# Performance work log

Measured on AMD Instinct MI355X. Metric: run time of the kernel, lower is better.

## Reference

```python
import jax, jax.numpy as jnp
import numpy as np
import math
from jax import lax

B, T, IN_DIM, D, H, L, OUT = 2, 2048, 128, 512, 8, 4, 128
HD = D // H
FF = int(4.0 * D)
NEG = -1e30  # stands in for -inf in the causal mask (identical softmax result)


def setup_inputs() -> dict:
    key = jax.random.key(0)
    ks = jax.random.split(key, 8)
    s = 0.02
    def p(k, shape):
        return jax.random.normal(k, shape, jnp.float32) * s
    return {
        "x": jax.random.normal(ks[0], (B, T, IN_DIM), jnp.float32),
        "Win": p(ks[1], (IN_DIM, D)), "bin_": jnp.zeros((D,), jnp.float32),
        "Wqkv": p(ks[2], (L, D, 3 * D)), "bqkv": jnp.zeros((L, 3 * D), jnp.float32),
        "Wo": p(ks[3], (L, D, D)), "bo": jnp.zeros((L, D), jnp.float32),
        "ln1_g": jnp.ones((L, D), jnp.float32), "ln1_b": jnp.zeros((L, D), jnp.float32),
        "Wf1": p(ks[4], (L, D, FF)), "bf1": jnp.zeros((L, FF), jnp.float32),
        "Wf2": p(ks[5], (L, FF, D)), "bf2": jnp.zeros((L, D), jnp.float32),
        "ln2_g": jnp.ones((L, D), jnp.float32), "ln2_b": jnp.zeros((L, D), jnp.float32),
        "lnf_g": jnp.ones((D,), jnp.float32), "lnf_b": jnp.zeros((D,), jnp.float32),
        "Wout": p(ks[6], (D, OUT)), "bout": jnp.zeros((OUT,), jnp.float32),
    }


def _layernorm(x, g, b, eps=1e-5):
    mu = jnp.mean(x, axis=-1, keepdims=True)
    var = jnp.mean(jnp.square(x - mu), axis=-1, keepdims=True)
    return (x - mu) * lax.rsqrt(var + eps) * g + b


def _sinusoidal_pe(t, d):
    pos = jnp.arange(t, dtype=jnp.float32)[:, None]
    div = jnp.exp(jnp.arange(0, d, 2, dtype=jnp.float32) * (-math.log(10000.0) / d))
    pe = jnp.zeros((t, d), jnp.float32)
    pe = pe.at[:, 0::2].set(jnp.sin(pos * div)).at[:, 1::2].set(jnp.cos(pos * div))
    return pe


def _alibi_bias():
    # ALiBi slopes (H=8 is a power of 2): start = 2**(-2**(-(log2(H)-3)))
    start = 2.0 ** (-(2.0 ** (-(math.log2(H) - 3.0))))
    slopes = jnp.array([start * (start ** i) for i in range(H)], jnp.float32)
    pos = jnp.arange(T)
    dist = jnp.triu(pos[None, :] - pos[:, None]).astype(jnp.float32)  # faithful: .triu() zeroes j<i
    bias = slopes[:, None, None] * dist  # [H,T,T]
    causal = jnp.triu(jnp.ones((T, T), bool), 1)
    return jnp.where(causal[None], NEG, bias)


def _forward(x, Win, bin_, Wqkv, bqkv, Wo, bo, ln1_g, ln1_b, Wf1, bf1, Wf2, bf2,
             ln2_g, ln2_b, lnf_g, lnf_b, Wout, bout):
    x = x @ Win + bin_                      # [B,T,D] project_in
    x = x + _sinusoidal_pe(T, D)            # internal time embedding
    bias = _alibi_bias()                    # [H,T,T]
    scale = 1.0 / math.sqrt(HD)

    def block(h, params):
        wqkv, bq, wo, bo_, g1, b1, wf1, bf1_, wf2, bf2_, g2, b2 = params
        y = _layernorm(h, g1, b1)
        qkv = y @ wqkv + bq                 # [B,T,3D]
        q, k, v = jnp.split(qkv, 3, axis=-1)
        def heads(t):
            return t.reshape(B, T, H, HD).transpose(0, 2, 1, 3)  # [B,H,T,HD]
        q, k, v = heads(q), heads(k), heads(v)
        logits = jnp.einsum('bhqd,bhkd->bhqk', q, k) * scale + bias[None]
        attn = jax.nn.softmax(logits, axis=-1)
        y = jnp.einsum('bhqk,bhkd->bhqd', attn, v)
        y = y.transpose(0, 2, 1, 3).reshape(B, T, D)
        h = h + (y @ wo + bo_)
        y = _layernorm(h, g2, b2)
        y = jax.nn.gelu(y @ wf1 + bf1_, approximate=False) @ wf2 + bf2_
        h = h + y
        return h, None

    x, _ = lax.scan(block, x, (Wqkv, bqkv, Wo, bo, ln1_g, ln1_b, Wf1, bf1, Wf2, bf2, ln2_g, ln2_b))
    x = _layernorm(x, lnf_g, lnf_b)         # final_norm
    return x @ Wout + bout                  # output head


def reference(x, Win, bin_, Wqkv, bqkv, Wo, bo, ln1_g, ln1_b, Wf1, bf1, Wf2, bf2,
              ln2_g, ln2_b, lnf_g, lnf_b, Wout, bout):
    return _forward(x, Win, bin_, Wqkv, bqkv, Wo, bo, ln1_g, ln1_b, Wf1, bf1,
                    Wf2, bf2, ln2_g, ln2_b, lnf_g, lnf_b, Wout, bout)
```

## Files before the change

kernel.cpp:

```cpp
#include <hip/hip_runtime.h>
#include <math.h>
#include <type_traits>
#include <utility>

#define TT 2048
typedef unsigned short u16;
typedef unsigned int u32;
typedef float f32x4 __attribute__((ext_vector_type(4)));
typedef float f32x16 __attribute__((ext_vector_type(16)));
typedef short s16x8 __attribute__((ext_vector_type(8)));
typedef __bf16 bf16x8 __attribute__((ext_vector_type(8)));
typedef __bf16 bf16x2 __attribute__((ext_vector_type(2)));
typedef u32 u32x4 __attribute__((ext_vector_type(4)));

enum { EPI_PE = 0, EPI_BF16 = 1, EPI_RES = 2, EPI_GELU = 3, EPI_OUTF = 4 };

template<typename V, typename = void> struct mfma_takes : std::false_type {};
template<typename V> struct mfma_takes<V, std::void_t<decltype(
    __builtin_amdgcn_mfma_f32_16x16x32_bf16(std::declval<V>(), std::declval<V>(),
                                            std::declval<f32x4>(), 0, 0, 0))>>
    : std::true_type {};

template<typename VA>
__device__ __forceinline__ f32x4 MFMA_t(VA a, VA b, f32x4 c) {
    if constexpr (mfma_takes<VA>::value) {
        return __builtin_amdgcn_mfma_f32_16x16x32_bf16(a, b, c, 0, 0, 0);
    } else {
        return __builtin_amdgcn_mfma_f32_16x16x32_bf16(
            __builtin_bit_cast(bf16x8, a), __builtin_bit_cast(bf16x8, b), c, 0, 0, 0);
    }
}

template<typename V, typename = void> struct mfma32_takes : std::false_type {};
template<typename V> struct mfma32_takes<V, std::void_t<decltype(
    __builtin_amdgcn_mfma_f32_32x32x16_bf16(std::declval<V>(), std::declval<V>(),
                                            std::declval<f32x16>(), 0, 0, 0))>>
    : std::true_type {};

template<typename VA>
__device__ __forceinline__ f32x16 MFMA32(VA a, VA b, f32x16 c) {
    if constexpr (mfma32_takes<VA>::value) {
        return __builtin_amdgcn_mfma_f32_32x32x16_bf16(a, b, c, 0, 0, 0);
    } else {
        return __builtin_amdgcn_mfma_f32_32x32x16_bf16(
            __builtin_bit_cast(bf16x8, a), __builtin_bit_cast(bf16x8, b), c, 0, 0, 0);
    }
}

__device__ __forceinline__ u16 f2b(float f) {
    u32 u = __float_as_uint(f);
    return (u16)((u + 0x7FFFu + ((u >> 16) & 1u)) >> 16);
}

__device__ __forceinline__ u32 pkbf(float a, float b) {
    bf16x2 t; t[0] = (__bf16)a; t[1] = (__bf16)b;
    return __builtin_bit_cast(u32, t);
}

__device__ __forceinline__ void gload16(const void* g, void* lds_base, int lds_byte_off) {
    __builtin_amdgcn_global_load_lds(
        (const __attribute__((address_space(1))) void*)g,
        (__attribute__((address_space(3))) void*)((char*)lds_base + lds_byte_off),
        16, 0, 0);
}

template<int EPI, int TM, int TN>
__global__ __launch_bounds__(256)
void k_gemm_mfma(const u16* __restrict__ A, const u16* __restrict__ Bt,
                 const float* __restrict__ bias, const float* __restrict__ Rf,
                 void* __restrict__ Cout, int M, int N, int K)
{
    constexpr int MF = TM / 32;
    constexpr int NF = TN / 32;
    __shared__ __attribute__((aligned(16))) u16 As[TM * 64];
    __shared__ __attribute__((aligned(16))) u16 Bs[TN * 64];
    const int tid = threadIdx.x;
    const int l = tid & 63, wv = tid >> 6;
    const int l15 = l & 15, lg = l >> 4;
    const int wr = wv >> 1, wc = wv & 1;
    const int row0 = blockIdx.y * TM, col0 = blockIdx.x * TN;

    f32x4 acc[MF][NF];
#pragma unroll
    for (int m = 0; m < MF; ++m)
#pragma unroll
        for (int n = 0; n < NF; ++n) acc[m][n] = (f32x4){0.f, 0.f, 0.f, 0.f};

    for (int kt = 0; kt < K; kt += 64) {
#pragma unroll
        for (int i = 0; i < TM / 32; ++i) {
            const int u = i * 256 + wv * 64 + l;
            const int ar = u >> 3, ac = u & 7;
            const int sc = (ac ^ (ar & 7)) << 3;
            const int off = __builtin_amdgcn_readfirstlane((i * 256 + wv * 64) * 16);
            gload16(A + (size_t)(row0 + ar) * K + kt + sc, As, off);
        }
#pragma unroll
        for (int i = 0; i < TN / 32; ++i) {
            const int u = i * 256 + wv * 64 + l;
            const int ar = u >> 3, ac = u & 7;
            const int sc = (ac ^ (ar & 7)) << 3;
            const int off = __builtin_amdgcn_readfirstlane((i * 256 + wv * 64) * 16);
            gload16(Bt + (size_t)(col0 + ar) * K + kt + sc, Bs, off);
        }
        __syncthreads();
        s16x8 af[MF][2], bf[NF][2];
#pragma unroll
        for (int m = 0; m < MF; ++m) {
            const int r = wr * (TM / 2) + m * 16 + l15;
#pragma unroll
            for (int s = 0; s < 2; ++s)
                af[m][s] = *(const s16x8*)(As + r * 64 + (((s * 4 + lg) ^ (r & 7)) << 3));
        }
#pragma unroll
        for (int n = 0; n < NF; ++n) {
            const int r = wc * (TN / 2) + n * 16 + l15;
#pragma unroll
            for (int s = 0; s < 2; ++s)
                bf[n][s] = *(const s16x8*)(Bs + r * 64 + (((s * 4 + lg) ^ (r & 7)) << 3));
        }
#pragma unroll
        for (int s = 0; s < 2; ++s)
#pragma unroll
            for (int m = 0; m < MF; ++m)
#pragma unroll
                for (int n = 0; n < NF; ++n)
                    acc[m][n] = MFMA_t(af[m][s], bf[n][s], acc[m][n]);
        __syncthreads();
    }

#pragma unroll
    for (int m = 0; m < MF; ++m)
#pragma unroll
        for (int rg = 0; rg < 4; ++rg) {
            const int row = row0 + wr * (TM / 2) + m * 16 + lg * 4 + rg;
#pragma unroll
            for (int n = 0; n < NF; ++n) {
                const int col = col0 + wc * (TN / 2) + n * 16 + l15;
                float v = acc[m][n][rg] + bias[col];
                const size_t idx = (size_t)row * N + col;
                if constexpr (EPI == EPI_PE) {
                    const int t = row & (TT - 1);
                    const float freq = __expf(-(float)(col & ~1) * 0.017988946039015984f);
                    const float ang = (float)t * freq;
                    v += (col & 1) ? cosf(ang) : sinf(ang);
                    ((float*)Cout)[idx] = v;
                } else if constexpr (EPI == EPI_BF16) {
                    ((u16*)Cout)[idx] = f2b(v);
                } else if constexpr (EPI == EPI_GELU) {
                    v = 0.5f * v * (1.f + erff(v * 0.7071067811865475f));
                    ((u16*)Cout)[idx] = f2b(v);
                } else if constexpr (EPI == EPI_RES) {
                    ((float*)Cout)[idx] = Rf[idx] + v;
                } else {
                    ((float*)Cout)[idx] = v;
                }
            }
        }
}

__global__ __launch_bounds__(256)
void k_ln(const float* __restrict__ X, const float* __restrict__ g,
          const float* __restrict__ b, u16* __restrict__ Y)
{
    const int lane = threadIdx.x & 63;
    const int row = blockIdx.x * 4 + (threadIdx.x >> 6);
    const float* x = X + (size_t)row * 512 + lane * 8;

    float4 v0 = *(const float4*)x;
    float4 v1 = *(const float4*)(x + 4);
    float vals[8] = {v0.x, v0.y, v0.z, v0.w, v1.x, v1.y, v1.z, v1.w};

    float s = 0.f;
#pragma unroll
    for (int i = 0; i < 8; ++i) s += vals[i];
#pragma unroll
    for (int off = 32; off >= 1; off >>= 1) s += __shfl_xor(s, off);
    const float mu = s * (1.f / 512.f);

    float sq = 0.f;
#pragma unroll
    for (int i = 0; i < 8; ++i) { float d = vals[i] - mu; sq += d * d; }
#pragma unroll
    for (int off = 32; off >= 1; off >>= 1) sq += __shfl_xor(sq, off);
    const float rs = rsqrtf(sq * (1.f / 512.f) + 1e-5f);

    const float* gp = g + lane * 8;
    const float* bp = b + lane * 8;
    float4 g0 = *(const float4*)gp, g1 = *(const float4*)(gp + 4);
    float4 b0 = *(const float4*)bp, b1 = *(const float4*)(bp + 4);
    float ga[8] = {g0.x, g0.y, g0.z, g0.w, g1.x, g1.y, g1.z, g1.w};
    float bb[8] = {b0.x, b0.y, b0.z, b0.w, b1.x, b1.y, b1.z, b1.w};

    u32 pk[4];
#pragma unroll
    for (int i = 0; i < 4; ++i) {
        float a0 = (vals[2 * i]     - mu) * rs * ga[2 * i]     + bb[2 * i];
        float a1 = (vals[2 * i + 1] - mu) * rs * ga[2 * i + 1] + bb[2 * i + 1];
        pk[i] = (u32)f2b(a0) | ((u32)f2b(a1) << 16);
    }
    *(uint4*)(Y + (size_t)row * 512 + lane * 8) = make_uint4(pk[0], pk[1], pk[2], pk[3]);
}

__global__ __launch_bounds__(256, 4)
void k_attn(const u16* __restrict__ qkv, const u16* __restrict__ Kf,
            const u16* __restrict__ Vf, u16* __restrict__ y)
{
    __shared__ float Om[4][32 * 65];
    __shared__ float Ml[4][32][2];
    const int tid = threadIdx.x;
    const int l = tid & 63, w = tid >> 6;
    const int l31 = l & 31, hi = l >> 5;
    const int bx = blockIdx.x;
    const int xcd = bx & 7, s = bx >> 3;
    const int bh = xcd * 2 + (s & 1);
    const int t_tile = 63 - (s >> 1);
    const int b = bh >> 3, hh = bh & 7;
    const int bT = b * TT, hh64 = hh * 64;

    const int qg = t_tile * 32 + l31;
    const int NT = (t_tile >> 1) + 1;

    f32x16 o[2] = {};
    float m = -1e30f, lsum = 0.f;

    if (w < NT) {
        s16x8 qf[4];
        {
            const u16* qsrc = qkv + (size_t)(bT + qg) * 1536 + hh64 + hi * 8;
#pragma unroll
            for (int dk = 0; dk < 4; ++dk) qf[dk] = *(const s16x8*)(qsrc + dk * 16);
        }
        const u16* kfb = Kf + ((size_t)bh * 8 + hi) * 2048 * 8;
        const u16* vfb = Vf + (((size_t)bh * 32) * 8 + hi) * 64 * 8;

        for (int g = w; g < NT; g += 4) {
            s16x8 kf[8];
#pragma unroll
            for (int nb = 0; nb < 2; ++nb)
#pragma unroll
                for (int dk = 0; dk < 4; ++dk)
                    kf[nb * 4 + dk] = *(const s16x8*)(
                        kfb + ((size_t)(dk * 2) * 2048 + g * 64 + nb * 32 + l31) * 8);

            f32x16 sA[2];
#pragma unroll
            for (int nb = 0; nb < 2; ++nb) {
                f32x16 acc = {};
#pragma unroll
                for (int dk = 0; dk < 4; ++dk) acc = MFMA32(kf[nb * 4 + dk], qf[dk], acc);
                sA[nb] = acc;
            }

            if (g == NT - 1) {
                const int kvb = g * 64, hi4 = hi * 4;
#pragma unroll
                for (int nb = 0; nb < 2; ++nb)
#pragma unroll
                    for (int r = 0; r < 16; ++r) {
                        const int kv = kvb + nb * 32 + (r & 3) + 8 * (r >> 2) + hi4;
                        sA[nb][r] = (kv > qg) ? -1e30f : sA[nb][r];
                    }
            }

            float tmp[16];
#pragma unroll
            for (int r = 0; r < 16; ++r) tmp[r] = fmaxf(sA[0][r], sA[1][r]);
#pragma unroll
            for (int st = 8; st >= 1; st >>= 1)
#pragma unroll
                for (int r = 0; r < 8; ++r)
                    if (r < st) tmp[r] = fmaxf(tmp[r], tmp[r + st]);
            float mt = fmaxf(tmp[0], __shfl_xor(tmp[0], 32));
            const bool grow = !__all(mt <= m);
            if (grow) {
                const float mn = fmaxf(m, mt);
                const float alpha = __expf((m - mn) * 0.125f);
                m = mn;
                lsum *= alpha;
#pragma unroll
                for (int dt = 0; dt < 2; ++dt)
#pragma unroll
                    for (int r = 0; r < 16; ++r) o[dt][r] *= alpha;
            }
            const float mc = -m * 0.125f;

            float p[2][16];
            float sum[16];
#pragma unroll
            for (int r = 0; r < 16; ++r) {
                p[0][r] = __expf(fmaf(sA[0][r], 0.125f, mc));
                p[1][r] = __expf(fmaf(sA[1][r], 0.125f, mc));
                sum[r] = p[0][r] + p[1][r];
            }
#pragma unroll
            for (int st = 8; st >= 1; st >>= 1)
#pragma unroll
                for (int r = 0; r < 8; ++r)
                    if (r < st) sum[r] += sum[r + st];
            float psum = sum[0] + __shfl_xor(sum[0], 32);
            lsum += psum;

            u32 pk2[2][8], sw2[2][8];
#pragma unroll
            for (int nb = 0; nb < 2; ++nb)
#pragma unroll
                for (int i = 0; i < 8; ++i) {
                    pk2[nb][i] = pkbf(p[nb][2 * i], p[nb][2 * i + 1]);
                    sw2[nb][i] = __shfl_xor(pk2[nb][i], 32);
                }
            s16x8 pa[4];
#pragma unroll
            for (int nb = 0; nb < 2; ++nb)
#pragma unroll
                for (int k16 = 0; k16 < 2; ++k16) {
                    const int i0 = k16 * 4;
                    u32 w0 = hi ? sw2[nb][i0 + 2] : pk2[nb][i0 + 0];
                    u32 w1 = hi ? sw2[nb][i0 + 3] : pk2[nb][i0 + 1];
                    u32 w2 = hi ? pk2[nb][i0 + 2] : sw2[nb][i0 + 0];
                    u32 w3 = hi ? pk2[nb][i0 + 3] : sw2[nb][i0 + 1];
                    u32x4 t4 = {w0, w1, w2, w3};
                    pa[nb * 2 + k16] = __builtin_bit_cast(s16x8, t4);
                }

#pragma unroll
            for (int dt = 0; dt < 2; ++dt) {
                f32x16 acc = o[dt];
#pragma unroll
                for (int ks = 0; ks < 4; ++ks)
                    acc = MFMA32(*(const s16x8*)(
                        vfb + (((size_t)g * 8 + ks * 2) * 64 + dt * 32 + l31) * 8),
                        pa[ks], acc);
                o[dt] = acc;
            }
        }
    }

#pragma unroll
    for (int dt = 0; dt < 2; ++dt)
#pragma unroll
        for (int r = 0; r < 16; ++r) {
            const int d = dt * 32 + (r & 3) + 8 * (r >> 2) + 4 * hi;
            Om[w][l31 * 65 + d] = o[dt][r];
        }
    Ml[w][l31][0] = m;
    Ml[w][l31][1] = lsum;
    __syncthreads();

    const int q = tid & 31, d0 = (tid >> 5) * 8;
    float m0 = Ml[0][q][0], m1 = Ml[1][q][0], m2 = Ml[2][q][0], m3 = Ml[3][q][0];
    const float mstar = fmaxf(fmaxf(m0, m1), fmaxf(m2, m3));
    float sc[4];
    sc[0] = __expf((m0 - mstar) * 0.125f);
    sc[1] = __expf((m1 - mstar) * 0.125f);
    sc[2] = __expf((m2 - mstar) * 0.125f);
    sc[3] = __expf((m3 - mstar) * 0.125f);
    const float lstar = sc[0] * Ml[0][q][1] + sc[1] * Ml[1][q][1]
                      + sc[2] * Ml[2][q][1] + sc[3] * Ml[3][q][1];
    float ov[8];
#pragma unroll
    for (int j = 0; j < 8; ++j) ov[j] = 0.f;
#pragma unroll
    for (int ww = 0; ww < 4; ++ww) {
        const float scw = sc[ww];
        const float* src = &Om[ww][q * 65 + d0];
#pragma unroll
        for (int j = 0; j < 8; ++j) ov[j] = fmaf(scw, src[j], ov[j]);
    }
    const float inv = 1.f / lstar;
    u32 pk[4];
#pragma unroll
    for (int i = 0; i < 4; ++i) pk[i] = pkbf(ov[2 * i] * inv, ov[2 * i + 1] * inv);
    u16* yp = y + (size_t)(bT + t_tile * 32 + q) * 512 + hh64 + d0;
    *(uint4*)yp = make_uint4(pk[0], pk[1], pk[2], pk[3]);
}

__global__ __launch_bounds__(256)
void k_kvf(const u16* __restrict__ big, u16* __restrict__ Kf, u16* __restrict__ Vf)
{
    __shared__ u16 TK[64][66];
    __shared__ u16 TV[64][66];
    const int tid = threadIdx.x;
    const int bh = blockIdx.x >> 5, g = blockIdx.x & 31;
    const int b = bh >> 3, hh = bh & 7;

#pragma unroll
    for (int i = 0; i < 2; ++i) {
        const int u = i * 256 + tid;
        const int r = u >> 3, c = u & 7;
        const u16* src = big + (size_t)(b * TT + g * 64 + r) * 1536 + 512 + hh * 64 + c * 8;
        s16x8 kv0 = *(const s16x8*)src;
        s16x8 vv0 = *(const s16x8*)(src + 512);
        u32x4 ka = __builtin_bit_cast(u32x4, kv0);
        u32x4 va = __builtin_bit_cast(u32x4, vv0);
        u32* dk_ = (u32*)&TK[r][c * 8];
        dk_[0] = ka[0]; dk_[1] = ka[1]; dk_[2] = ka[2]; dk_[3] = ka[3];
        u32* dv_ = (u32*)&TV[r][c * 8];
        dv_[0] = va[0]; dv_[1] = va[1]; dv_[2] = va[2]; dv_[3] = va[3];
    }
    __syncthreads();

#pragma unroll
    for (int i = 0; i < 2; ++i) {
        const int u = i * 256 + tid;
        const int c2 = u >> 6, t = u & 63;
        const u32* s4 = (const u32*)&TK[t][c2 * 8];
        *(uint4*)(Kf + (((size_t)bh * 8 + c2) * 2048 + g * 64 + t) * 8)
            = make_uint4(s4[0], s4[1], s4[2], s4[3]);
    }
#pragma unroll
    for (int i = 0; i < 2; ++i) {
        const int u = i * 256 + tid;
        const int cc = u >> 6, d = u & 63;
        u32 pk[4];
#pragma unroll
        for (int jp = 0; jp < 4; ++jp)
            pk[jp] = (u32)TV[cc * 8 + 2 * jp][d] | ((u32)TV[cc * 8 + 2 * jp + 1][d] << 16);
        *(uint4*)(Vf + ((((size_t)bh * 32 + g) * 8 + cc) * 64 + d) * 8)
            = make_uint4(pk[0], pk[1], pk[2], pk[3]);
    }
}

__global__ __launch_bounds__(256)
void k_wt_all(const float* __restrict__ Wqkv, const float* __restrict__ Wo,
              const float* __restrict__ Wf1, const float* __restrict__ Wf2,
              const float* __restrict__ Win, const float* __restrict__ Wout,
              u16* __restrict__ WqkvT, u16* __restrict__ WoT,
              u16* __restrict__ Wf1T, u16* __restrict__ Wf2T,
              u16* __restrict__ WinT, u16* __restrict__ WoutT)
{
    __shared__ float T[64][65];
    const int tid = threadIdx.x;
    int id = blockIdx.x;
    const float* W; u16* Wt; int K, N;
    if (id < 3072) {
        const int lyr = id / 768, sub = id - lyr * 768;
        if (sub < 192)      { W = Wqkv + (size_t)lyr * 512 * 1536; Wt = WqkvT + (size_t)lyr * 512 * 1536; K = 512;  N = 1536; id = sub; }
        else if (sub < 256) { W = Wo   + (size_t)lyr * 512 * 512;  Wt = WoT   + (size_t)lyr * 512 * 512;  K = 512;  N = 512;  id = sub - 192; }
        else if (sub < 512) { W = Wf1  + (size_t)lyr * 512 * 2048; Wt = Wf1T  + (size_t)lyr * 512 * 2048; K = 512;  N = 2048; id = sub - 256; }
        else                { W = Wf2  + (size_t)lyr * 2048 * 512; Wt = Wf2T  + (size_t)lyr * 2048 * 512; K = 2048; N = 512;  id = sub - 512; }
    } else if (id < 3088)   { W = Win;  Wt = WinT;  K = 128; N = 512; id -= 3072; }
    else                    { W = Wout; Wt = WoutT; K = 512; N = 128; id -= 3088; }
    const int nt = N >> 6;
    const int ktile = id / nt, ntile = id - ktile * nt;
    const int kb = ktile * 64, nb = ntile * 64;
#pragma unroll
    for (int i = 0; i < 4; ++i) {
        const int r = i * 16 + (tid >> 4), c = (tid & 15) * 4;
        const float4 v = *(const float4*)&W[(size_t)(kb + r) * N + nb + c];
        T[r][c] = v.x; T[r][c + 1] = v.y; T[r][c + 2] = v.z; T[r][c + 3] = v.w;
    }
    __syncthreads();
    const int n = tid >> 2, k0 = (tid & 3) * 16;
    u32 pk[8];
#pragma unroll
    for (int i = 0; i < 8; ++i)
        pk[i] = pkbf(T[k0 + 2 * i][n], T[k0 + 2 * i + 1][n]);
    uint4* dst = (uint4*)(Wt + (size_t)(nb + n) * K + kb + k0);
    dst[0] = make_uint4(pk[0], pk[1], pk[2], pk[3]);
    dst[1] = make_uint4(pk[4], pk[5], pk[6], pk[7]);
}

__global__ __launch_bounds__(256)
void k_f2b(const float* __restrict__ x, u16* __restrict__ xb)
{
    const int g = blockIdx.x * 256 + threadIdx.x;
    const float4* s = (const float4*)(x + (size_t)g * 8);
    float4 a = s[0], c = s[1];
    u32 pk[4] = {
        (u32)f2b(a.x) | ((u32)f2b(a.y) << 16), (u32)f2b(a.z) | ((u32)f2b(a.w) << 16),
        (u32)f2b(c.x) | ((u32)f2b(c.y) << 16), (u32)f2b(c.z) | ((u32)f2b(c.w) << 16)};
    *(uint4*)(xb + (size_t)g * 8) = make_uint4(pk[0], pk[1], pk[2], pk[3]);
}

extern "C" void kernel_launch(void* const* d_in, const int* in_sizes, int n_in,
                              void* d_out, int out_size, void* d_ws, size_t ws_size,
                              hipStream_t stream)
{
    const float* x    = (const float*)d_in[0];
    const float* Win  = (const float*)d_in[1];
    const float* bin_ = (const float*)d_in[2];
    const float* Wqkv = (const float*)d_in[3];
    const float* bqkv = (const float*)d_in[4];
    const float* Wo   = (const float*)d_in[5];
    const float* bo   = (const float*)d_in[6];
    const float* ln1g = (const float*)d_in[7];
    const float* ln1b = (const float*)d_in[8];
    const float* Wf1  = (const float*)d_in[9];
    const float* bf1  = (const float*)d_in[10];
    const float* Wf2  = (const float*)d_in[11];
    const float* bf2  = (const float*)d_in[12];
    const float* ln2g = (const float*)d_in[13];
    const float* ln2b = (const float*)d_in[14];
    const float* lnfg = (const float*)d_in[15];
    const float* lnfb = (const float*)d_in[16];
    const float* Wout = (const float*)d_in[17];
    const float* bout = (const float*)d_in[18];
    float* out = (float*)d_out;

    const int M = 4096;
    char* ws = (char*)d_ws;
    float* h    = (float*)(ws + 0);
    u16*   y    = (u16*)(ws + 8388608);
    u16*   big  = (u16*)(ws + 12582912);
    u16*   Kf   = (u16*)(ws + 29360128);
    u16*   Vf   = (u16*)(ws + 33554432);
    u16*   xb   = big;
    u16*   WinT  = (u16*)(ws + 37748736);
    u16*   WoutT = (u16*)(ws + 37879808);
    u16*   WqkvT = (u16*)(ws + 38010880);
    u16*   WoT   = (u16*)(ws + 44302336);
    u16*   Wf1T  = (u16*)(ws + 46399488);
    u16*   Wf2T  = (u16*)(ws + 54788096);

    dim3 blk(256);

    k_f2b<<<256, blk, 0, stream>>>(x, xb);
    k_wt_all<<<3104, blk, 0, stream>>>(Wqkv, Wo, Wf1, Wf2, Win, Wout,
                                       WqkvT, WoT, Wf1T, Wf2T, WinT, WoutT);

    k_gemm_mfma<EPI_PE, 64, 64><<<dim3(8, 64), blk, 0, stream>>>(
        xb, WinT, bin_, nullptr, h, M, 512, 128);

    for (int lyr = 0; lyr < 4; ++lyr) {
        k_ln<<<1024, blk, 0, stream>>>(h, ln1g + lyr * 512, ln1b + lyr * 512, y);
        k_gemm_mfma<EPI_BF16, 64, 128><<<dim3(12, 64), blk, 0, stream>>>(
            y, WqkvT + (size_t)lyr * 512 * 1536, bqkv + lyr * 1536, nullptr, big, M, 1536, 512);
        k_kvf<<<512, blk, 0, stream>>>(big, Kf, Vf);
        k_attn<<<1024, blk, 0, stream>>>(big, Kf, Vf, y);
        k_gemm_mfma<EPI_RES, 64, 64><<<dim3(8, 64), blk, 0, stream>>>(
            y, WoT + (size_t)lyr * 512 * 512, bo + lyr * 512, h, h, M, 512, 512);
        k_ln<<<1024, blk, 0, stream>>>(h, ln2g + lyr * 512, ln2b + lyr * 512, y);
        k_gemm_mfma<EPI_GELU, 64, 128><<<dim3(16, 64), blk, 0, stream>>>(
            y, Wf1T + (size_t)lyr * 512 * 2048, bf1 + lyr * 2048, nullptr, big, M, 2048, 512);
        k_gemm_mfma<EPI_RES, 64, 64><<<dim3(8, 64), blk, 0, stream>>>(
            big, Wf2T + (size_t)lyr * 2048 * 512, bf2 + lyr * 512, h, h, M, 512, 2048);
    }

    k_ln<<<1024, blk, 0, stream>>>(h, lnfg, lnfb, y);
    k_gemm_mfma<EPI_OUTF, 64, 64><<<dim3(2, 64), blk, 0, stream>>>(
        y, WoutT, bout, nullptr, out, M, 128, 512);
}
```

Measured before the change: 479.1 us.

## Restructure attention to share double-buffered LDS K/V tiles across two query waves

Each attention block now handles 64 queries with two waves instead of 32 queries split across four waves over the KV range. K and V tiles are loaded into a double-buffered LDS area with direct global-to-LDS loads, so both waves reuse them and the next tile is prefetched during compute. This removes the cross-wave softmax merge through shared memory and the redundant per-wave global K/V loads. In exchange there is less KV-dimension parallelism per query tile, half as many blocks, and a barrier on every KV step.

```diff
diff --git a/kernel.cpp b/kernel.cpp
--- a/kernel.cpp
+++ b/kernel.cpp
@@ -202,177 +202,170 @@
     *(uint4*)(Y + (size_t)row * 512 + lane * 8) = make_uint4(pk[0], pk[1], pk[2], pk[3]);
 }
 
-__global__ __launch_bounds__(256, 4)
+__global__ __launch_bounds__(128, 4)
 void k_attn(const u16* __restrict__ qkv, const u16* __restrict__ Kf,
             const u16* __restrict__ Vf, u16* __restrict__ y)
 {
-    __shared__ float Om[4][32 * 65];
-    __shared__ float Ml[4][32][2];
+    __shared__ __attribute__((aligned(16))) u16 KV[2 * 8192];
     const int tid = threadIdx.x;
     const int l = tid & 63, w = tid >> 6;
     const int l31 = l & 31, hi = l >> 5;
     const int bx = blockIdx.x;
     const int xcd = bx & 7, s = bx >> 3;
     const int bh = xcd * 2 + (s & 1);
-    const int t_tile = 63 - (s >> 1);
+    const int t_tile = 31 - (s >> 1);
     const int b = bh >> 3, hh = bh & 7;
     const int bT = b * TT, hh64 = hh * 64;
 
-    const int qg = t_tile * 32 + l31;
-    const int NT = (t_tile >> 1) + 1;
+    const int qg = t_tile * 64 + w * 32 + l31;
+    const int NT = t_tile + 1;
+
+    const u16* KfB = Kf + (size_t)bh * 8 * 2048 * 8;
+    const u16* VfB = Vf + (size_t)bh * 32 * 8 * 64 * 8;
+
+    auto STAGE = [&](int g, int buf) {
+        const int bb = buf * 16384;
+#pragma unroll
+        for (int i = 0; i < 4; ++i) {
+            const int u = i * 128 + tid;
+            const int c = u >> 6, t = u & 63;
+            const int off = __builtin_amdgcn_readfirstlane(bb + (i * 128 + w * 64) * 16);
+            gload16(KfB + ((size_t)c * 2048 + g * 64 + t) * 8, (void*)KV, off);
+            gload16(VfB + ((size_t)(g * 8 + c) * 64 + t) * 8, (void*)KV, off + 8192);
+        }
+    };
+
+    STAGE(0, 0);
+
+    s16x8 qf[4];
+    {
+        const u16* qsrc = qkv + (size_t)(bT + qg) * 1536 + hh64 + hi * 8;
+#pragma unroll
+        for (int dk = 0; dk < 4; ++dk) qf[dk] = *(const s16x8*)(qsrc + dk * 16);
+    }
 
     f32x16 o[2] = {};
     float m = -1e30f, lsum = 0.f;
 
-    if (w < NT) {
-        s16x8 qf[4];
-        {
-            const u16* qsrc = qkv + (size_t)(bT + qg) * 1536 + hh64 + hi * 8;
-#pragma unroll
-            for (int dk = 0; dk < 4; ++dk) qf[dk] = *(const s16x8*)(qsrc + dk * 16);
-        }
-        const u16* kfb = Kf + ((size_t)bh * 8 + hi) * 2048 * 8;
-        const u16* vfb = Vf + (((size_t)bh * 32) * 8 + hi) * 64 * 8;
-
-        for (int g = w; g < NT; g += 4) {
-            s16x8 kf[8];
+    for (int kb = 0; kb < NT; ++kb) {
+        const int cur = kb & 1;
+        if (kb + 1 < NT) {
+            STAGE(kb + 1, cur ^ 1);
+            asm volatile("s_waitcnt vmcnt(8)" ::: "memory");
+        } else {
+            asm volatile("s_waitcnt vmcnt(0)" ::: "memory");
+        }
+        __builtin_amdgcn_s_barrier();
+        __builtin_amdgcn_sched_barrier(0);
+
+        const u16* kb_ = KV + cur * 8192;
+        const u16* vb_ = kb_ + 4096;
+
+        f32x16 sA[2];
+#pragma unroll
+        for (int nb = 0; nb < 2; ++nb) {
+            f32x16 acc = {};
+#pragma unroll
+            for (int dk = 0; dk < 4; ++dk)
+                acc = MFMA32(*(const s16x8*)(
+                    kb_ + ((dk * 2 + hi) * 64 + nb * 32 + l31) * 8), qf[dk], acc);
+            sA[nb] = acc;
+        }
+
+        if (kb == NT - 1) {
+            const int kvb = kb * 64, hi4 = hi * 4;
 #pragma unroll
             for (int nb = 0; nb < 2; ++nb)
 #pragma unroll
-                for (int dk = 0; dk < 4; ++dk)
-                    kf[nb * 4 + dk] = *(const s16x8*)(
-                        kfb + ((size_t)(dk * 2) * 2048 + g * 64 + nb * 32 + l31) * 8);
-
-            f32x16 sA[2];
-#pragma unroll
-            for (int nb = 0; nb < 2; ++nb) {
-                f32x16 acc = {};
-#pragma unroll
-                for (int dk = 0; dk < 4; ++dk) acc = MFMA32(kf[nb * 4 + dk], qf[dk], acc);
-                sA[nb] = acc;
+                for (int r = 0; r < 16; ++r) {
+                    const int kv = kvb + nb * 32 + (r & 3) + 8 * (r >> 2) + hi4;
+                    sA[nb][r] = (kv > qg) ? -1e30f : sA[nb][r];
+                }
+        }
+
+        float tmp[16];
+#pragma unroll
+        for (int r = 0; r < 16; ++r) tmp[r] = fmaxf(sA[0][r], sA[1][r]);
+#pragma unroll
+        for (int st = 8; st >= 1; st >>= 1)
+#pragma unroll
+            for (int r = 0; r < 8; ++r)
+                if (r < st) tmp[r] = fmaxf(tmp[r], tmp[r + st]);
+        float mt = fmaxf(tmp[0], __shfl_xor(tmp[0], 32));
+        const bool grow = !__all(mt <= m);
+        if (grow) {
+            const float mn = fmaxf(m, mt);
+            const float alpha = __expf((m - mn) * 0.125f);
+            m = mn;
+            lsum *= alpha;
+#pragma unroll
+            for (int dt = 0; dt < 2; ++dt)
+#pragma unroll
+                for (int r = 0; r < 16; ++r) o[dt][r] *= alpha;
+        }
+        const float mc = -m * 0.125f;
+
+        float p[2][16];
+        float sum[16];
+#pragma unroll
+        for (int r = 0; r < 16; ++r) {
+            p[0][r] = __expf(fmaf(sA[0][r], 0.125f, mc));
+            p[1][r] = __expf(fmaf(sA[1][r], 0.125f, mc));
+            sum[r] = p[0][r] + p[1][r];
+        }
+#pragma unroll
+        for (int st = 8; st >= 1; st >>= 1)
+#pragma unroll
+            for (int r = 0; r < 8; ++r)
+                if (r < st) sum[r] += sum[r + st];
+        float psum = sum[0] + __shfl_xor(sum[0], 32);
+        lsum += psum;
+
+        u32 pk2[2][8], sw2[2][8];
+#pragma unroll
+        for (int nb = 0; nb < 2; ++nb)
+#pragma unroll
+            for (int i = 0; i < 8; ++i) {
+                pk2[nb][i] = pkbf(p[nb][2 * i], p[nb][2 * i + 1]);
+                sw2[nb][i] = __shfl_xor(pk2[nb][i], 32);
             }
-
-            if (g == NT - 1) {
-                const int kvb = g * 64, hi4 = hi * 4;
-#pragma unroll
-                for (int nb = 0; nb < 2; ++nb)
-#pragma unroll
-                    for (int r = 0; r < 16; ++r) {
-                        const int kv = kvb + nb * 32 + (r & 3) + 8 * (r >> 2) + hi4;
-                        sA[nb][r] = (kv > qg) ? -1e30f : sA[nb][r];
-                    }
+        s16x8 pa[4];
+#pragma unroll
+        for (int nb = 0; nb < 2; ++nb)
+#pragma unroll
+            for (int k16 = 0; k16 < 2; ++k16) {
+                const int i0 = k16 * 4;
+                u32 w0 = hi ? sw2[nb][i0 + 2] : pk2[nb][i0 + 0];
+                u32 w1 = hi ? sw2[nb][i0 + 3] : pk2[nb][i0 + 1];
+                u32 w2 = hi ? pk2[nb][i0 + 2] : sw2[nb][i0 + 0];
+                u32 w3 = hi ? pk2[nb][i0 + 3] : sw2[nb][i0 + 1];
+                u32x4 t4 = {w0, w1, w2, w3};
+                pa[nb * 2 + k16] = __builtin_bit_cast(s16x8, t4);
             }
 
-            float tmp[16];
-#pragma unroll
-            for (int r = 0; r < 16; ++r) tmp[r] = fmaxf(sA[0][r], sA[1][r]);
-#pragma unroll
-            for (int st = 8; st >= 1; st >>= 1)
-#pragma unroll
-                for (int r = 0; r < 8; ++r)
-                    if (r < st) tmp[r] = fmaxf(tmp[r], tmp[r + st]);
-            float mt = fmaxf(tmp[0], __shfl_xor(tmp[0], 32));
-            const bool grow = !__all(mt <= m);
-            if (grow) {
-                const float mn = fmaxf(m, mt);
-                const float alpha = __expf((m - mn) * 0.125f);
-                m = mn;
-                lsum *= alpha;
-#pragma unroll
-                for (int dt = 0; dt < 2; ++dt)
-#pragma unroll
-                    for (int r = 0; r < 16; ++r) o[dt][r] *= alpha;
-            }
-            const float mc = -m * 0.125f;
-
-            float p[2][16];
-            float sum[16];
-#pragma unroll
-            for (int r = 0; r < 16; ++r) {
-                p[0][r] = __expf(fmaf(sA[0][r], 0.125f, mc));
-                p[1][r] = __expf(fmaf(sA[1][r], 0.125f, mc));
-                sum[r] = p[0][r] + p[1][r];
-            }
-#pragma unroll
-            for (int st = 8; st >= 1; st >>= 1)
-#pragma unroll
-                for (int r = 0; r < 8; ++r)
-                    if (r < st) sum[r] += sum[r + st];
-            float psum = sum[0] + __shfl_xor(sum[0], 32);
-            lsum += psum;
-
-            u32 pk2[2][8], sw2[2][8];
-#pragma unroll
-            for (int nb = 0; nb < 2; ++nb)
-#pragma unroll
-                for (int i = 0; i < 8; ++i) {
-                    pk2[nb][i] = pkbf(p[nb][2 * i], p[nb][2 * i + 1]);
-                    sw2[nb][i] = __shfl_xor(pk2[nb][i], 32);
-                }
-            s16x8 pa[4];
-#pragma unroll
-            for (int nb = 0; nb < 2; ++nb)
-#pragma unroll
-                for (int k16 = 0; k16 < 2; ++k16) {
-                    const int i0 = k16 * 4;
-                    u32 w0 = hi ? sw2[nb][i0 + 2] : pk2[nb][i0 + 0];
-                    u32 w1 = hi ? sw2[nb][i0 + 3] : pk2[nb][i0 + 1];
-                    u32 w2 = hi ? pk2[nb][i0 + 2] : sw2[nb][i0 + 0];
-                    u32 w3 = hi ? pk2[nb][i0 + 3] : sw2[nb][i0 + 1];
-                    u32x4 t4 = {w0, w1, w2, w3};
-                    pa[nb * 2 + k16] = __builtin_bit_cast(s16x8, t4);
-                }
-
-#pragma unroll
-            for (int dt = 0; dt < 2; ++dt) {
-                f32x16 acc = o[dt];
-#pragma unroll
-                for (int ks = 0; ks < 4; ++ks)
-                    acc = MFMA32(*(const s16x8*)(
-                        vfb + (((size_t)g * 8 + ks * 2) * 64 + dt * 32 + l31) * 8),
-                        pa[ks], acc);
-                o[dt] = acc;
-            }
-        }
-    }
-
+#pragma unroll
+        for (int dt = 0; dt < 2; ++dt) {
+            f32x16 acc = o[dt];
+#pragma unroll
+            for (int ks = 0; ks < 4; ++ks)
+                acc = MFMA32(*(const s16x8*)(
+                    vb_ + ((ks * 2 + hi) * 64 + dt * 32 + l31) * 8), pa[ks], acc);
+            o[dt] = acc;
+        }
+
+        __builtin_amdgcn_sched_barrier(0);
+        __builtin_amdgcn_s_barrier();
+    }
+
+    const float inv = 1.f / lsum;
+    u16* yrow = y + (size_t)(bT + qg) * 512 + hh64;
 #pragma unroll
     for (int dt = 0; dt < 2; ++dt)
 #pragma unroll
-        for (int r = 0; r < 16; ++r) {
-            const int d = dt * 32 + (r & 3) + 8 * (r >> 2) + 4 * hi;
-            Om[w][l31 * 65 + d] = o[dt][r];
-        }
-    Ml[w][l31][0] = m;
-    Ml[w][l31][1] = lsum;
-    __syncthreads();
-
-    const int q = tid & 31, d0 = (tid >> 5) * 8;
-    float m0 = Ml[0][q][0], m1 = Ml[1][q][0], m2 = Ml[2][q][0], m3 = Ml[3][q][0];
-    const float mstar = fmaxf(fmaxf(m0, m1), fmaxf(m2, m3));
-    float sc[4];
-    sc[0] = __expf((m0 - mstar) * 0.125f);
-    sc[1] = __expf((m1 - mstar) * 0.125f);
-    sc[2] = __expf((m2 - mstar) * 0.125f);
-    sc[3] = __expf((m3 - mstar) * 0.125f);
-    const float lstar = sc[0] * Ml[0][q][1] + sc[1] * Ml[1][q][1]
-                      + sc[2] * Ml[2][q][1] + sc[3] * Ml[3][q][1];
-    float ov[8];
-#pragma unroll
-    for (int j = 0; j < 8; ++j) ov[j] = 0.f;
-#pragma unroll
-    for (int ww = 0; ww < 4; ++ww) {
-        const float scw = sc[ww];
-        const float* src = &Om[ww][q * 65 + d0];
-#pragma unroll
-        for (int j = 0; j < 8; ++j) ov[j] = fmaf(scw, src[j], ov[j]);
-    }
-    const float inv = 1.f / lstar;
-    u32 pk[4];
-#pragma unroll
-    for (int i = 0; i < 4; ++i) pk[i] = pkbf(ov[2 * i] * inv, ov[2 * i + 1] * inv);
-    u16* yp = y + (size_t)(bT + t_tile * 32 + q) * 512 + hh64 + d0;
-    *(uint4*)yp = make_uint4(pk[0], pk[1], pk[2], pk[3]);
+        for (int i = 0; i < 8; ++i) {
+            const int d = dt * 32 + ((2 * i) & 3) + 8 * (i >> 1) + 4 * hi;
+            *(u32*)(yrow + d) = pkbf(o[dt][2 * i] * inv, o[dt][2 * i + 1] * inv);
+        }
 }
 
 __global__ __launch_bounds__(256)
@@ -527,7 +520,7 @@
         k_gemm_mfma<EPI_BF16, 64, 128><<<dim3(12, 64), blk, 0, stream>>>(
             y, WqkvT + (size_t)lyr * 512 * 1536, bqkv + lyr * 1536, nullptr, big, M, 1536, 512);
         k_kvf<<<512, blk, 0, stream>>>(big, Kf, Vf);
-        k_attn<<<1024, blk, 0, stream>>>(big, Kf, Vf, y);
+        k_attn<<<512, dim3(128), 0, stream>>>(big, Kf, Vf, y);
         k_gemm_mfma<EPI_RES, 64, 64><<<dim3(8, 64), blk, 0, stream>>>(
             y, WoT + (size_t)lyr * 512 * 512, bo + lyr * 512, h, h, M, 512, 512);
         k_ln<<<1024, blk, 0, stream>>>(h, ln2g + lyr * 512, ln2b + lyr * 512, y);
```

After: 530.8 us. +10.8%, slower.

## Double-buffer GEMM LDS tiles with async prefetch of next K-slice

Applied to the files above, without the earlier changes.

Splits the GEMM shared-memory tiles into two buffers and issues the global-to-LDS loads for the next K tile before computing on the current one. Manual vmcnt waits replace the full __syncthreads, so each wave only waits for the loads of the current stage. This aims to hide global memory latency behind the MFMA work, at the cost of twice the LDS, which may reduce occupancy. The vmcnt counts are hardcoded per tile configuration, which makes correctness depend on the LP value matching the number of loads actually issued.

```diff
diff --git a/kernel.cpp b/kernel.cpp
--- a/kernel.cpp
+++ b/kernel.cpp
@@ -72,8 +72,9 @@
 {
     constexpr int MF = TM / 32;
     constexpr int NF = TN / 32;
-    __shared__ __attribute__((aligned(16))) u16 As[TM * 64];
-    __shared__ __attribute__((aligned(16))) u16 Bs[TN * 64];
+    constexpr int LP = TM / 32 + TN / 32;
+    __shared__ __attribute__((aligned(16))) u16 As[2][TM * 64];
+    __shared__ __attribute__((aligned(16))) u16 Bs[2][TN * 64];
     const int tid = threadIdx.x;
     const int l = tid & 63, wv = tid >> 6;
     const int l15 = l & 15, lg = l >> 4;
@@ -86,14 +87,14 @@
 #pragma unroll
         for (int n = 0; n < NF; ++n) acc[m][n] = (f32x4){0.f, 0.f, 0.f, 0.f};
 
-    for (int kt = 0; kt < K; kt += 64) {
+    auto STAGE = [&](int kt, int buf) {
 #pragma unroll
         for (int i = 0; i < TM / 32; ++i) {
             const int u = i * 256 + wv * 64 + l;
             const int ar = u >> 3, ac = u & 7;
             const int sc = (ac ^ (ar & 7)) << 3;
             const int off = __builtin_amdgcn_readfirstlane((i * 256 + wv * 64) * 16);
-            gload16(A + (size_t)(row0 + ar) * K + kt + sc, As, off);
+            gload16(A + (size_t)(row0 + ar) * K + kt + sc, As[buf], off);
         }
 #pragma unroll
         for (int i = 0; i < TN / 32; ++i) {
@@ -101,23 +102,41 @@
             const int ar = u >> 3, ac = u & 7;
             const int sc = (ac ^ (ar & 7)) << 3;
             const int off = __builtin_amdgcn_readfirstlane((i * 256 + wv * 64) * 16);
-            gload16(Bt + (size_t)(col0 + ar) * K + kt + sc, Bs, off);
-        }
-        __syncthreads();
+            gload16(Bt + (size_t)(col0 + ar) * K + kt + sc, Bs[buf], off);
+        }
+    };
+
+    const int nk = K >> 6;
+    STAGE(0, 0);
+
+    for (int t = 0; t < nk; ++t) {
+        const int cur = t & 1;
+        if (t + 1 < nk) {
+            STAGE((t + 1) << 6, cur ^ 1);
+            if constexpr (LP == 4)
+                asm volatile("s_waitcnt vmcnt(4)" ::: "memory");
+            else
+                asm volatile("s_waitcnt vmcnt(6)" ::: "memory");
+        } else {
+            asm volatile("s_waitcnt vmcnt(0)" ::: "memory");
+        }
+        __builtin_amdgcn_s_barrier();
+        __builtin_amdgcn_sched_barrier(0);
+
         s16x8 af[MF][2], bf[NF][2];
 #pragma unroll
         for (int m = 0; m < MF; ++m) {
             const int r = wr * (TM / 2) + m * 16 + l15;
 #pragma unroll
             for (int s = 0; s < 2; ++s)
-                af[m][s] = *(const s16x8*)(As + r * 64 + (((s * 4 + lg) ^ (r & 7)) << 3));
+                af[m][s] = *(const s16x8*)(As[cur] + r * 64 + (((s * 4 + lg) ^ (r & 7)) << 3));
         }
 #pragma unroll
         for (int n = 0; n < NF; ++n) {
             const int r = wc * (TN / 2) + n * 16 + l15;
 #pragma unroll
             for (int s = 0; s < 2; ++s)
-                bf[n][s] = *(const s16x8*)(Bs + r * 64 + (((s * 4 + lg) ^ (r & 7)) << 3));
+                bf[n][s] = *(const s16x8*)(Bs[cur] + r * 64 + (((s * 4 + lg) ^ (r & 7)) << 3));
         }
 #pragma unroll
         for (int s = 0; s < 2; ++s)
@@ -126,7 +145,9 @@
 #pragma unroll
                 for (int n = 0; n < NF; ++n)
                     acc[m][n] = MFMA_t(af[m][s], bf[n][s], acc[m][n]);
-        __syncthreads();
+
+        __builtin_amdgcn_sched_barrier(0);
+        __builtin_amdgcn_s_barrier();
     }
 
 #pragma unroll
```

Result: slower. 490.7 us (+2.4%).
